# Performance work log

Measured on AMD Instinct MI355X. Metric: run time of the kernel, lower is better.

## Reference

```python
import jax, jax.numpy as jnp
import numpy as np

OUTPUT_SIZE = (7, 7)
SPATIAL_SCALE = 0.25
SAMPLING_RATIO = 2


def setup_inputs() -> dict:
    key = jax.random.key(0)
    k1, k2, k3, k4, k5 = jax.random.split(key, 5)
    N, C, H, W = 2, 256, 200, 304
    R = 1000
    features = jax.random.normal(k1, (N, C, H, W), dtype=jnp.float32)
    # Boxes in IMAGE coordinates (image ~ 800x1216 since spatial_scale=0.25)
    img_h, img_w = H / SPATIAL_SCALE, W / SPATIAL_SCALE
    batch_idx = jax.random.randint(k2, (R,), 0, N).astype(jnp.float32)
    x1 = jax.random.uniform(k3, (R,), minval=0.0, maxval=img_w * 0.8)
    y1 = jax.random.uniform(k4, (R,), minval=0.0, maxval=img_h * 0.8)
    wh = jax.random.uniform(k5, (R, 2), minval=16.0, maxval=256.0)
    x2 = jnp.minimum(x1 + wh[:, 0], img_w - 1.0)
    y2 = jnp.minimum(y1 + wh[:, 1], img_h - 1.0)
    boxes = jnp.stack([batch_idx, x1, y1, x2, y2], axis=1).astype(jnp.float32)
    return {"features": features, "boxes": boxes}


def _axis_interp(coord, size):
    """torchvision bilinear_interpolate clamping along one axis.
    coord: float sample positions. Returns (low_idx, high_idx, frac, valid)."""
    valid = (coord >= -1.0) & (coord <= size)
    c = jnp.maximum(coord, 0.0)
    low_raw = jnp.floor(c).astype(jnp.int32)
    at_edge = low_raw >= size - 1
    low = jnp.where(at_edge, size - 1, low_raw)
    high = jnp.where(at_edge, size - 1, low_raw + 1)
    frac = jnp.where(at_edge, 0.0, c - low_raw.astype(c.dtype))
    return low, high, frac, valid


def roi_align(features, boxes, output_size, spatial_scale, sampling_ratio):
    N, C, H, W = features.shape
    PH, PW = output_size
    G = sampling_ratio
    b = boxes[:, 0].astype(jnp.int32)                      # [R]
    x1 = boxes[:, 1] * spatial_scale
    y1 = boxes[:, 2] * spatial_scale
    x2 = boxes[:, 3] * spatial_scale
    y2 = boxes[:, 4] * spatial_scale
    roi_w = jnp.maximum(x2 - x1, 1.0)
    roi_h = jnp.maximum(y2 - y1, 1.0)
    bin_h = roi_h / PH
    bin_w = roi_w / PW
    off = (jnp.arange(G, dtype=jnp.float32) + 0.5) / G     # [G] sample offsets in bin
    # per-axis sample coords: ys [R,PH,G], xs [R,PW,G]
    ys = y1[:, None, None] + (jnp.arange(PH, dtype=jnp.float32)[None, :, None] + off[None, None, :]) * bin_h[:, None, None]
    xs = x1[:, None, None] + (jnp.arange(PW, dtype=jnp.float32)[None, :, None] + off[None, None, :]) * bin_w[:, None, None]
    yl, yh, fy, vy = _axis_interp(ys, H)
    xl, xh, fx, vx = _axis_interp(xs, W)
    feat = features.transpose(0, 2, 3, 1)                  # [N,H,W,C]
    bb = b[:, None, None, None, None]                      # broadcast to [R,PH,G,PW,G]
    Y = lambda idx: idx[:, :, :, None, None]
    X = lambda idx: idx[:, None, None, :, :]
    # four corner gathers -> [R,PH,G,PW,G,C]
    v_ll = feat[bb, Y(yl), X(xl)]
    v_lh = feat[bb, Y(yl), X(xh)]
    v_hl = feat[bb, Y(yh), X(xl)]
    v_hh = feat[bb, Y(yh), X(xh)]
    fy_b = fy[:, :, :, None, None, None]
    fx_b = fx[:, None, None, :, :, None]
    interp = ((1 - fy_b) * (1 - fx_b) * v_ll + (1 - fy_b) * fx_b * v_lh
              + fy_b * (1 - fx_b) * v_hl + fy_b * fx_b * v_hh)
    valid = (vy[:, :, :, None, None] & vx[:, None, None, :, :])[..., None]
    interp = jnp.where(valid, interp, 0.0)
    pooled = interp.mean(axis=(2, 4))                      # avg over G*G samples -> [R,PH,PW,C]
    return pooled.transpose(0, 3, 1, 2)                    # [R,C,PH,PW]


def reference(features, boxes):
    return roi_align(features, boxes, OUTPUT_SIZE, SPATIAL_SCALE, SAMPLING_RATIO)
```

## Files before the change

### kernel.cpp

```cpp
#include <hip/hip_runtime.h>
#include <hip/hip_bf16.h>


constexpr int N_B  = 2;
constexpr int C_CH = 256;
constexpr int H_F  = 200;
constexpr int W_F  = 304;
constexpr int HW   = H_F * W_F;
constexpr int PH   = 7;
constexpr int PW   = 7;
constexpr int CELLS = PH * PW;
constexpr int CSTRIDE = 56;
constexpr int NXCD = 8;
constexpr float SCALE = 0.25f;

typedef float  v4f __attribute__((ext_vector_type(4)));

static __device__ __forceinline__ unsigned short f2bf(float f) {
    __hip_bfloat16 h = __float2bfloat16(f);
    return *reinterpret_cast<unsigned short*>(&h);
}
static __device__ __forceinline__ float blo(unsigned int u) {
    return __uint_as_float(u << 16);
}
static __device__ __forceinline__ float bhi(unsigned int u) {
    return __uint_as_float(u & 0xffff0000u);
}

__global__ __launch_bounds__(1024) void sort_rois(
    const float* __restrict__ boxes, unsigned int* __restrict__ perm, int R)
{
    int t = threadIdx.x;
    if (R > 1024) {
        for (int i = t; i < R; i += 1024) perm[i] = (unsigned int)i;
        return;
    }
    __shared__ unsigned int k[1024];
    unsigned int key = 0xFFFFFFFFu;
    if (t < R) {
        const float* box = boxes + t * 5;
        int b  = (int)box[0];
        float yc = (box[2] + box[4]) * 0.5f * SCALE;
        float xc = (box[1] + box[3]) * 0.5f * SCALE;
        int yq = min(max((int)yc, 0), H_F - 1);
        int xq = min(max((int)xc, 0), W_F - 1);
        int stripe = yq >> 4;
        int xs = (stripe & 1) ? (W_F - 1 - xq) : xq;
        unsigned int s = ((unsigned int)b << 13) | ((unsigned int)stripe << 9)
                       | (unsigned int)xs;
        key = (s << 10) | (unsigned int)t;
    }
    k[t] = key;
    __syncthreads();
#pragma unroll 1
    for (int size = 2; size <= 1024; size <<= 1) {
#pragma unroll 1
        for (int stride = size >> 1; stride > 0; stride >>= 1) {
            int j = t ^ stride;
            if (j > t) {
                unsigned int a = k[t], c = k[j];
                bool up = ((t & size) == 0);
                if ((a > c) == up) { k[t] = c; k[j] = a; }
            }
            __syncthreads();
        }
    }
    if (t < R) perm[t] = k[t] & 1023u;
}

__global__ __launch_bounds__(256) void transpose_nchw_nhwc_bf16(
    const float* __restrict__ in, unsigned short* __restrict__ out)
{
    __shared__ float tile[64][65];
    int tx = blockIdx.x * 64;
    int ty = blockIdx.y * 64;
    int n  = blockIdx.z;
    const float* ip = in  + (size_t)n * C_CH * HW;
    unsigned short* op = out + (size_t)n * HW * C_CH;

    int w4 = threadIdx.x & 15;
    int cr = threadIdx.x >> 4;
#pragma unroll
    for (int p = 0; p < 4; ++p) {
        int c = p * 16 + cr;
        v4f v = __builtin_nontemporal_load(
            (const v4f*)&ip[(size_t)(ty + c) * HW + tx + 4 * w4]);
        tile[c][4 * w4 + 0] = v.x;
        tile[c][4 * w4 + 1] = v.y;
        tile[c][4 * w4 + 2] = v.z;
        tile[c][4 * w4 + 3] = v.w;
    }
    __syncthreads();
    int cq = threadIdx.x & 15;
    int hr = threadIdx.x >> 4;
#pragma unroll
    for (int p = 0; p < 4; ++p) {
        int hw = p * 16 + hr;
        ushort4 v;
        v.x = f2bf(tile[4 * cq + 0][hw]);
        v.y = f2bf(tile[4 * cq + 1][hw]);
        v.z = f2bf(tile[4 * cq + 2][hw]);
        v.w = f2bf(tile[4 * cq + 3][hw]);
        *(ushort4*)&op[(size_t)(tx + hw) * C_CH + ty + 4 * cq] = v;
    }
}

static __device__ __forceinline__ void acc8(
    float* acc, uint4 ll, uint4 lh, uint4 hl, uint4 hh,
    float fxx, float fyy, float w)
{
#define ACC_PAIR(C, I0, I1)                                                   \
    { float a = blo(ll.C), b = blo(lh.C), c = blo(hl.C), d = blo(hh.C);       \
      float lo = a + fxx * (b - a), hi = c + fxx * (d - c);                   \
      acc[I0] += w * (lo + fyy * (hi - lo)); }                                \
    { float a = bhi(ll.C), b = bhi(lh.C), c = bhi(hl.C), d = bhi(hh.C);       \
      float lo = a + fxx * (b - a), hi = c + fxx * (d - c);                   \
      acc[I1] += w * (lo + fyy * (hi - lo)); }
    ACC_PAIR(x, 0, 1)
    ACC_PAIR(y, 2, 3)
    ACC_PAIR(z, 4, 5)
    ACC_PAIR(w, 6, 7)
#undef ACC_PAIR
}

__global__ __launch_bounds__(512) void roi_gather_nhwc(
    const unsigned short* __restrict__ feat_nhwc,
    const float* __restrict__ boxes,
    const unsigned int* __restrict__ perm,
    float* __restrict__ out, int R)
{
    __shared__ alignas(16) float lds[C_CH * CSTRIDE];
    int pos = blockIdx.x;
    if (pos >= R) return;
    if ((R & (NXCD - 1)) == 0) {
        int cpx = R / NXCD;
        pos = (pos & (NXCD - 1)) * cpx + (pos >> 3);
    }
    int r = (int)perm[pos];
    if (r >= R) return;

    int tid = threadIdx.x;
    int grp = tid >> 5;
    int ln  = tid & 31;
    int swz = ln & 7;

    const float* box = boxes + r * 5;
    int   b  = (int)box[0];
    float x1 = box[1] * SCALE;
    float y1 = box[2] * SCALE;
    float x2 = box[3] * SCALE;
    float y2 = box[4] * SCALE;
    float bin_w = fmaxf(x2 - x1, 1.0f) * (1.0f / PW);
    float bin_h = fmaxf(y2 - y1, 1.0f) * (1.0f / PH);

    const unsigned short* fb = feat_nhwc + (size_t)b * HW * C_CH + 8 * ln;

    for (int cell = grp; cell < CELLS; cell += 16) {
        int ph = cell / PW;
        int pw = cell - ph * PW;

        int   yl[2], yh[2]; float fy[2], vy[2];
#pragma unroll
        for (int iy = 0; iy < 2; ++iy) {
            float y = y1 + ((float)ph + (iy ? 0.75f : 0.25f)) * bin_h;
            vy[iy] = (y >= -1.0f && y <= (float)H_F) ? 1.0f : 0.0f;
            float cy = fmaxf(y, 0.0f);
            int ylr = (int)floorf(cy);
            bool e = (ylr >= H_F - 1);
            yl[iy] = e ? H_F - 1 : ylr;
            yh[iy] = e ? H_F - 1 : ylr + 1;
            fy[iy] = e ? 0.0f : cy - (float)ylr;
        }
        int   xl[2], xh[2]; float fx[2], vx[2];
#pragma unroll
        for (int ix = 0; ix < 2; ++ix) {
            float x = x1 + ((float)pw + (ix ? 0.75f : 0.25f)) * bin_w;
            vx[ix] = (x >= -1.0f && x <= (float)W_F) ? 1.0f : 0.0f;
            float cx = fmaxf(x, 0.0f);
            int xlr = (int)floorf(cx);
            bool e = (xlr >= W_F - 1);
            xl[ix] = e ? W_F - 1 : xlr;
            xh[ix] = e ? W_F - 1 : xlr + 1;
            fx[ix] = e ? 0.0f : cx - (float)xlr;
        }

        float acc[8] = {0.f, 0.f, 0.f, 0.f, 0.f, 0.f, 0.f, 0.f};

#pragma unroll
        for (int iy = 0; iy < 2; ++iy) {
            const unsigned short* rl = fb + (size_t)(yl[iy] * W_F) * C_CH;
            const unsigned short* rh = fb + (size_t)(yh[iy] * W_F) * C_CH;
            uint4 l0 = *(const uint4*)(rl + (size_t)xl[0] * C_CH);
            uint4 l1 = *(const uint4*)(rl + (size_t)xh[0] * C_CH);
            uint4 l2 = *(const uint4*)(rl + (size_t)xl[1] * C_CH);
            uint4 l3 = *(const uint4*)(rl + (size_t)xh[1] * C_CH);
            uint4 h0 = *(const uint4*)(rh + (size_t)xl[0] * C_CH);
            uint4 h1 = *(const uint4*)(rh + (size_t)xh[0] * C_CH);
            uint4 h2 = *(const uint4*)(rh + (size_t)xl[1] * C_CH);
            uint4 h3 = *(const uint4*)(rh + (size_t)xh[1] * C_CH);
            acc8(acc, l0, l1, h0, h1, fx[0], fy[iy], vy[iy] * vx[0]);
            acc8(acc, l2, l3, h2, h3, fx[1], fy[iy], vy[iy] * vx[1]);
        }

        int cellx = cell ^ swz;
#pragma unroll
        for (int j = 0; j < 8; ++j)
            lds[(8 * ln + j) * CSTRIDE + cellx] = acc[j] * 0.25f;
    }
    __syncthreads();

    float4* dst = (float4*)(out + (size_t)r * (C_CH * CELLS));
    for (int q = tid; q < (C_CH * CELLS) / 4; q += 512) {
        int w0 = 4 * q;
        float4 v;
        {
            int c = w0 / 49, ce = w0 - 49 * c;
            v.x = lds[c * CSTRIDE + (ce ^ ((c >> 3) & 7))];
        }
        {
            int wv = w0 + 1; int c = wv / 49, ce = wv - 49 * c;
            v.y = lds[c * CSTRIDE + (ce ^ ((c >> 3) & 7))];
        }
        {
            int wv = w0 + 2; int c = wv / 49, ce = wv - 49 * c;
            v.z = lds[c * CSTRIDE + (ce ^ ((c >> 3) & 7))];
        }
        {
            int wv = w0 + 3; int c = wv / 49, ce = wv - 49 * c;
            v.w = lds[c * CSTRIDE + (ce ^ ((c >> 3) & 7))];
        }
        dst[q] = v;
    }
}

__global__ __launch_bounds__(256) void roi_align_fallback(
    const float* __restrict__ feat,
    const float* __restrict__ boxes,
    float* __restrict__ out, int total)
{
    int idx = blockIdx.x * 256 + threadIdx.x;
    if (idx >= total) return;
    int pw = idx % PW;
    int t  = idx / PW;
    int ph = t % PH;
    t /= PH;
    int c = t & (C_CH - 1);
    int r = t >> 8;

    const float* box = boxes + r * 5;
    int   b  = (int)box[0];
    float x1 = box[1] * SCALE;
    float y1 = box[2] * SCALE;
    float x2 = box[3] * SCALE;
    float y2 = box[4] * SCALE;
    float bin_w = fmaxf(x2 - x1, 1.0f) * (1.0f / PW);
    float bin_h = fmaxf(y2 - y1, 1.0f) * (1.0f / PH);
    const float* fp = feat + ((size_t)b * C_CH + c) * HW;

    float acc = 0.0f;
#pragma unroll
    for (int iy = 0; iy < 2; ++iy) {
        float y = y1 + ((float)ph + (iy ? 0.75f : 0.25f)) * bin_h;
        bool vy = (y >= -1.0f) && (y <= (float)H_F);
        float cy = fmaxf(y, 0.0f);
        int ylr = (int)floorf(cy);
        int yl, yh; float fyv;
        if (ylr >= H_F - 1) { yl = H_F - 1; yh = H_F - 1; fyv = 0.0f; }
        else                { yl = ylr;     yh = ylr + 1; fyv = cy - (float)ylr; }
#pragma unroll
        for (int ix = 0; ix < 2; ++ix) {
            float x = x1 + ((float)pw + (ix ? 0.75f : 0.25f)) * bin_w;
            bool vx = (x >= -1.0f) && (x <= (float)W_F);
            float cx = fmaxf(x, 0.0f);
            int xlr = (int)floorf(cx);
            int xlv, xhv; float fxv;
            if (xlr >= W_F - 1) { xlv = W_F - 1; xhv = W_F - 1; fxv = 0.0f; }
            else                { xlv = xlr;     xhv = xlr + 1; fxv = cx - (float)xlr; }
            if (vy && vx) {
                const float* rl = fp + yl * W_F;
                const float* rh = fp + yh * W_F;
                float vll = rl[xlv], vlh = rl[xhv], vhl = rh[xlv], vhh = rh[xhv];
                float vlo = vll + fxv * (vlh - vll);
                float vhi = vhl + fxv * (vhh - vhl);
                acc += vlo + fyv * (vhi - vlo);
            }
        }
    }
    out[idx] = acc * 0.25f;
}

extern "C" void kernel_launch(void* const* d_in, const int* in_sizes, int n_in,
                              void* d_out, int out_size, void* d_ws, size_t ws_size,
                              hipStream_t stream) {
    const float* feat  = (const float*)d_in[0];
    const float* boxes = (const float*)d_in[1];
    float* out = (float*)d_out;
    int R = in_sizes[1] / 5;

    size_t need_nhwc = (size_t)N_B * C_CH * HW * sizeof(unsigned short);
    size_t perm_off  = (need_nhwc + 255) & ~(size_t)255;
    size_t need      = perm_off + (size_t)((R > 1024 ? R : 1024)) * sizeof(unsigned int);
    if (ws_size >= need) {
        unsigned short* nhwc = (unsigned short*)d_ws;
        unsigned int*   perm = (unsigned int*)((char*)d_ws + perm_off);
        sort_rois<<<1, 1024, 0, stream>>>(boxes, perm, R);
        dim3 tg(HW / 64, C_CH / 64, N_B);
        transpose_nchw_nhwc_bf16<<<tg, 256, 0, stream>>>(feat, nhwc);
        roi_gather_nhwc<<<R, 512, 0, stream>>>(nhwc, boxes, perm, out, R);
    } else {
        int total = out_size;
        roi_align_fallback<<<(total + 255) / 256, 256, 0, stream>>>(feat, boxes, out, total);
    }
}
```

Measured before the change: 230.3 us.

## Software-pipeline corner gathers across cells and write output directly without LDS

The gather loop now prefetches the next cell's 16 corner loads into registers while interpolating the current cell, aiming to hide global load latency. The LDS staging buffer, block barrier and the coalesced float4 write-out are removed; each thread writes its 8 channel results straight to global memory with a stride of 49 floats. This frees the large shared allocation, which may let more blocks fit per CU, but it adds register pressure from the double-buffered uint4 arrays and makes the output stores scattered and uncoalesced.

```diff
diff --git a/kernel.cpp b/kernel.cpp
--- a/kernel.cpp
+++ b/kernel.cpp
@@ -10,7 +10,6 @@
 constexpr int PH   = 7;
 constexpr int PW   = 7;
 constexpr int CELLS = PH * PW;
-constexpr int CSTRIDE = 56;
 constexpr int NXCD = 8;
 constexpr float SCALE = 0.25f;
 
@@ -105,6 +104,55 @@
     }
 }
 
+struct Geom {
+    int   yl[2], yh[2]; float fy[2], vy[2];
+    int   xl[2], xh[2]; float fx[2], vx[2];
+};
+
+static __device__ __forceinline__ void geom_cell(
+    Geom& g, int cell, float x1, float y1, float bin_w, float bin_h)
+{
+    int ph = cell / PW;
+    int pw = cell - ph * PW;
+#pragma unroll
+    for (int iy = 0; iy < 2; ++iy) {
+        float y = y1 + ((float)ph + (iy ? 0.75f : 0.25f)) * bin_h;
+        g.vy[iy] = (y >= -1.0f && y <= (float)H_F) ? 1.0f : 0.0f;
+        float cy = fmaxf(y, 0.0f);
+        int ylr = (int)floorf(cy);
+        bool e = (ylr >= H_F - 1);
+        g.yl[iy] = e ? H_F - 1 : ylr;
+        g.yh[iy] = e ? H_F - 1 : ylr + 1;
+        g.fy[iy] = e ? 0.0f : cy - (float)ylr;
+    }
+#pragma unroll
+    for (int ix = 0; ix < 2; ++ix) {
+        float x = x1 + ((float)pw + (ix ? 0.75f : 0.25f)) * bin_w;
+        g.vx[ix] = (x >= -1.0f && x <= (float)W_F) ? 1.0f : 0.0f;
+        float cx = fmaxf(x, 0.0f);
+        int xlr = (int)floorf(cx);
+        bool e = (xlr >= W_F - 1);
+        g.xl[ix] = e ? W_F - 1 : xlr;
+        g.xh[ix] = e ? W_F - 1 : xlr + 1;
+        g.fx[ix] = e ? 0.0f : cx - (float)xlr;
+    }
+}
+
+static __device__ __forceinline__ void load_half(
+    uint4 t[8], const unsigned short* fb, const Geom& g, int iy)
+{
+    const unsigned short* rl = fb + (size_t)(g.yl[iy] * W_F) * C_CH;
+    const unsigned short* rh = fb + (size_t)(g.yh[iy] * W_F) * C_CH;
+    t[0] = *(const uint4*)(rl + (size_t)g.xl[0] * C_CH);
+    t[1] = *(const uint4*)(rl + (size_t)g.xh[0] * C_CH);
+    t[2] = *(const uint4*)(rl + (size_t)g.xl[1] * C_CH);
+    t[3] = *(const uint4*)(rl + (size_t)g.xh[1] * C_CH);
+    t[4] = *(const uint4*)(rh + (size_t)g.xl[0] * C_CH);
+    t[5] = *(const uint4*)(rh + (size_t)g.xh[0] * C_CH);
+    t[6] = *(const uint4*)(rh + (size_t)g.xl[1] * C_CH);
+    t[7] = *(const uint4*)(rh + (size_t)g.xh[1] * C_CH);
+}
+
 static __device__ __forceinline__ void acc8(
     float* acc, uint4 ll, uint4 lh, uint4 hl, uint4 hh,
     float fxx, float fyy, float w)
@@ -123,13 +171,19 @@
 #undef ACC_PAIR
 }
 
+static __device__ __forceinline__ void math_half(
+    float acc[8], const uint4 t[8], const Geom& g, int iy)
+{
+    acc8(acc, t[0], t[1], t[4], t[5], g.fx[0], g.fy[iy], g.vy[iy] * g.vx[0]);
+    acc8(acc, t[2], t[3], t[6], t[7], g.fx[1], g.fy[iy], g.vy[iy] * g.vx[1]);
+}
+
 __global__ __launch_bounds__(512) void roi_gather_nhwc(
     const unsigned short* __restrict__ feat_nhwc,
     const float* __restrict__ boxes,
     const unsigned int* __restrict__ perm,
     float* __restrict__ out, int R)
 {
-    __shared__ alignas(16) float lds[C_CH * CSTRIDE];
     int pos = blockIdx.x;
     if (pos >= R) return;
     if ((R & (NXCD - 1)) == 0) {
@@ -142,7 +196,6 @@
     int tid = threadIdx.x;
     int grp = tid >> 5;
     int ln  = tid & 31;
-    int swz = ln & 7;
 
     const float* box = boxes + r * 5;
     int   b  = (int)box[0];
@@ -154,82 +207,33 @@
     float bin_h = fmaxf(y2 - y1, 1.0f) * (1.0f / PH);
 
     const unsigned short* fb = feat_nhwc + (size_t)b * HW * C_CH + 8 * ln;
-
+    float* ob = out + (size_t)r * (C_CH * CELLS) + (size_t)(8 * ln) * CELLS;
+
+    Geom g;
+    geom_cell(g, grp, x1, y1, bin_w, bin_h);
+    uint4 t0[8], t1[8];
+    load_half(t0, fb, g, 0);
+    load_half(t1, fb, g, 1);
+
+#pragma unroll 1
     for (int cell = grp; cell < CELLS; cell += 16) {
-        int ph = cell / PW;
-        int pw = cell - ph * PW;
-
-        int   yl[2], yh[2]; float fy[2], vy[2];
-#pragma unroll
-        for (int iy = 0; iy < 2; ++iy) {
-            float y = y1 + ((float)ph + (iy ? 0.75f : 0.25f)) * bin_h;
-            vy[iy] = (y >= -1.0f && y <= (float)H_F) ? 1.0f : 0.0f;
-            float cy = fmaxf(y, 0.0f);
-            int ylr = (int)floorf(cy);
-            bool e = (ylr >= H_F - 1);
-            yl[iy] = e ? H_F - 1 : ylr;
-            yh[iy] = e ? H_F - 1 : ylr + 1;
-            fy[iy] = e ? 0.0f : cy - (float)ylr;
-        }
-        int   xl[2], xh[2]; float fx[2], vx[2];
-#pragma unroll
-        for (int ix = 0; ix < 2; ++ix) {
-            float x = x1 + ((float)pw + (ix ? 0.75f : 0.25f)) * bin_w;
-            vx[ix] = (x >= -1.0f && x <= (float)W_F) ? 1.0f : 0.0f;
-            float cx = fmaxf(x, 0.0f);
-            int xlr = (int)floorf(cx);
-            bool e = (xlr >= W_F - 1);
-            xl[ix] = e ? W_F - 1 : xlr;
-            xh[ix] = e ? W_F - 1 : xlr + 1;
-            fx[ix] = e ? 0.0f : cx - (float)xlr;
-        }
+        int  nxt  = cell + 16;
+        bool has  = (nxt < CELLS);
+        Geom gn;
+        if (has) geom_cell(gn, nxt, x1, y1, bin_w, bin_h);
 
         float acc[8] = {0.f, 0.f, 0.f, 0.f, 0.f, 0.f, 0.f, 0.f};
-
-#pragma unroll
-        for (int iy = 0; iy < 2; ++iy) {
-            const unsigned short* rl = fb + (size_t)(yl[iy] * W_F) * C_CH;
-            const unsigned short* rh = fb + (size_t)(yh[iy] * W_F) * C_CH;
-            uint4 l0 = *(const uint4*)(rl + (size_t)xl[0] * C_CH);
-            uint4 l1 = *(const uint4*)(rl + (size_t)xh[0] * C_CH);
-            uint4 l2 = *(const uint4*)(rl + (size_t)xl[1] * C_CH);
-            uint4 l3 = *(const uint4*)(rl + (size_t)xh[1] * C_CH);
-            uint4 h0 = *(const uint4*)(rh + (size_t)xl[0] * C_CH);
-            uint4 h1 = *(const uint4*)(rh + (size_t)xh[0] * C_CH);
-            uint4 h2 = *(const uint4*)(rh + (size_t)xl[1] * C_CH);
-            uint4 h3 = *(const uint4*)(rh + (size_t)xh[1] * C_CH);
-            acc8(acc, l0, l1, h0, h1, fx[0], fy[iy], vy[iy] * vx[0]);
-            acc8(acc, l2, l3, h2, h3, fx[1], fy[iy], vy[iy] * vx[1]);
-        }
-
-        int cellx = cell ^ swz;
+        math_half(acc, t0, g, 0);
+        if (has) load_half(t0, fb, gn, 0);
+        math_half(acc, t1, g, 1);
+        if (has) load_half(t1, fb, gn, 1);
+
+        float* o = ob + cell;
 #pragma unroll
         for (int j = 0; j < 8; ++j)
-            lds[(8 * ln + j) * CSTRIDE + cellx] = acc[j] * 0.25f;
-    }
-    __syncthreads();
-
-    float4* dst = (float4*)(out + (size_t)r * (C_CH * CELLS));
-    for (int q = tid; q < (C_CH * CELLS) / 4; q += 512) {
-        int w0 = 4 * q;
-        float4 v;
-        {
-            int c = w0 / 49, ce = w0 - 49 * c;
-            v.x = lds[c * CSTRIDE + (ce ^ ((c >> 3) & 7))];
-        }
-        {
-            int wv = w0 + 1; int c = wv / 49, ce = wv - 49 * c;
-            v.y = lds[c * CSTRIDE + (ce ^ ((c >> 3) & 7))];
-        }
-        {
-            int wv = w0 + 2; int c = wv / 49, ce = wv - 49 * c;
-            v.z = lds[c * CSTRIDE + (ce ^ ((c >> 3) & 7))];
-        }
-        {
-            int wv = w0 + 3; int c = wv / 49, ce = wv - 49 * c;
-            v.w = lds[c * CSTRIDE + (ce ^ ((c >> 3) & 7))];
-        }
-        dst[q] = v;
+            o[j * CELLS] = acc[j] * 0.25f;
+
+        g = gn;
     }
 }
 
```

Result: slower. 272.9 us (+18.5%).
